# Kernel tuning notes

Hardware: AMD Instinct MI355X
Metric: run time of the kernel (lower is better)

## Reference

```python
import jax, jax.numpy as jnp
import numpy as np

NUM_NODES = 100000
NUM_RELS = 200
DIM = 128
NUM_EDGES = 600000


def setup_inputs() -> dict:
    key = jax.random.key(0)
    ks = jax.random.split(key, 12)
    xav = lambda k, shp: jax.random.uniform(k, shp, jnp.float32, -1.0, 1.0) * jnp.sqrt(6.0 / (shp[0] + shp[1]))
    return {
        'edge_index': jax.random.randint(ks[0], (2, NUM_EDGES), 0, NUM_NODES),
        'edge_type': jax.random.randint(ks[1], (NUM_EDGES,), 0, NUM_RELS),
        'edge_weight': jax.random.uniform(ks[2], (NUM_EDGES,), jnp.float32),
        'node_emb': xav(ks[3], (NUM_NODES, DIM)),
        'rel_emb': xav(ks[4], (NUM_RELS, DIM)),
        'W0': xav(ks[5], (DIM, DIM)),
        'Wself0': xav(ks[6], (DIM, DIM)),
        'Wrel0': xav(ks[7], (DIM, DIM)),
        'W1': xav(ks[8], (DIM, DIM)),
        'Wself1': xav(ks[9], (DIM, DIM)),
        'Wrel1': xav(ks[10], (DIM, DIM)),
    }


def comp_sub(x_src, r):
    return x_src - r


def compgcn_conv(x, rel, edge_index, edge_type, edge_weight, W, Wself, Wrel):
    src, dst = edge_index[0], edge_index[1]
    # edge-wise gather + composition: [E, D]
    msg = comp_sub(x[src], rel[edge_type])
    msg = msg * edge_weight[:, None]
    # scatter-add aggregation to destination nodes: [N, D]
    agg = jax.ops.segment_sum(msg, dst, num_segments=x.shape[0])
    x_out = agg @ W + x @ Wself
    rel_out = rel @ Wrel
    return x_out, rel_out


def reference(edge_index, edge_type, edge_weight, node_emb, rel_emb,
              W0, Wself0, Wrel0, W1, Wself1, Wrel1):
    # layer 0
    x, rel = compgcn_conv(node_emb, rel_emb, edge_index, edge_type, edge_weight,
                          W0, Wself0, Wrel0)
    # inter-layer nonlinearity (dropout is identity in eval mode)
    x = jax.nn.relu(x)
    rel = jax.nn.relu(rel)
    # layer 1 (last layer: no relu/dropout after)
    x, rel = compgcn_conv(x, rel, edge_index, edge_type, edge_weight,
                          W1, Wself1, Wrel1)
    return x, rel
```

## Files before the change

### kernel.cpp

```cpp
#include <hip/hip_runtime.h>

#define DD 128

typedef __attribute__((ext_vector_type(8))) short bf16x8;
typedef __attribute__((ext_vector_type(4))) float f32x4;

__device__ __forceinline__ float b2f(unsigned short u) {
    return __uint_as_float(((unsigned)u) << 16);
}
__device__ __forceinline__ unsigned short f2b(float f) {
    unsigned u = __float_as_uint(f);
    unsigned r = (u + 0x7FFFu + ((u >> 16) & 1u)) >> 16;
    return (unsigned short)r;
}


__global__ __launch_bounds__(256) void zero_kernel(int4* __restrict__ p, int n4) {
    int i = blockIdx.x * 256 + threadIdx.x;
    if (i < n4) p[i] = make_int4(0, 0, 0, 0);
}


__global__ __launch_bounds__(256) void scan1_kernel(const int* __restrict__ cnt8,
                                                    int* __restrict__ startv,
                                                    int* __restrict__ bsum, int n) {
    int i = blockIdx.x * 256 + threadIdx.x;
    int v = 0;
    if (i < n) {
#pragma unroll
        for (int p = 0; p < 8; ++p) v += cnt8[p * n + i];
    }
    int lane = threadIdx.x & 63, wid = threadIdx.x >> 6;
    int incl = v;
#pragma unroll
    for (int o = 1; o < 64; o <<= 1) {
        int t = __shfl_up(incl, o);
        if (lane >= o) incl += t;
    }
    __shared__ int wsum[4];
    __shared__ int wpre[4];
    if (lane == 63) wsum[wid] = incl;
    __syncthreads();
    if (threadIdx.x == 0) {
        int s = 0;
        for (int w2 = 0; w2 < 4; ++w2) { wpre[w2] = s; s += wsum[w2]; }
        bsum[blockIdx.x] = s;
    }
    __syncthreads();
    if (i < n) startv[i] = incl - v + wpre[wid];
}

__global__ __launch_bounds__(512) void scan2_kernel(int* bsum, int nb) {
    int i = threadIdx.x;
    int v = (i < nb) ? bsum[i] : 0;
    int lane = threadIdx.x & 63, wid = threadIdx.x >> 6;
    int incl = v;
#pragma unroll
    for (int o = 1; o < 64; o <<= 1) {
        int t = __shfl_up(incl, o);
        if (lane >= o) incl += t;
    }
    __shared__ int wsum[8];
    __shared__ int wpre[8];
    if (lane == 63) wsum[wid] = incl;
    __syncthreads();
    if (threadIdx.x == 0) {
        int s = 0;
        for (int w2 = 0; w2 < 8; ++w2) { wpre[w2] = s; s += wsum[w2]; }
    }
    __syncthreads();
    if (i < nb) bsum[i] = incl - v + wpre[wid];
}

__global__ __launch_bounds__(256) void scan3_kernel(int* startv,
                                                    const int* __restrict__ cnt8,
                                                    int* __restrict__ cursor8,
                                                    const int* __restrict__ bsum,
                                                    int n, int E) {
    int i = blockIdx.x * 256 + threadIdx.x;
    if (i < n) {
        int s = startv[i] + bsum[i >> 8];
        startv[i] = s;
        int run = s;
#pragma unroll
        for (int p = 0; p < 8; ++p) {
            cursor8[p * n + i] = run;
            run += cnt8[p * n + i];
        }
    } else if (i == n) {
        startv[n] = E;
    }
}

__global__ __launch_bounds__(256) void fill_kernel(const int* __restrict__ ei,
                                                   const int* __restrict__ ety,
                                                   const float* __restrict__ ew,
                                                   int* cursor8,
                                                   uint2* __restrict__ csre,
                                                   int E, int n) {
    int e = blockIdx.x * 256 + threadIdx.x;
    if (e >= E) return;
    int p = blockIdx.x & 7;
    int dst = ei[E + e];
    int pos = atomicAdd(&cursor8[p * n + dst], 1);
    uint2 rec;
    rec.x = ((unsigned)ei[e]) | (((unsigned)ety[e]) << 20);
    rec.y = __float_as_uint(ew[e]);
    __builtin_nontemporal_store(*(unsigned long long*)&rec,
                                (unsigned long long*)&csre[pos]);
}


__global__ __launch_bounds__(256) void prep_hist_kernel(
    const float* __restrict__ x0, unsigned short* __restrict__ xb, int bx, int n4x,
    const float* __restrict__ r0, unsigned short* __restrict__ r0b, int br, int n4r,
    const float* __restrict__ W0, const float* __restrict__ Ws0,
    const float* __restrict__ W1, const float* __restrict__ Ws1,
    const float* __restrict__ Wr0, const float* __restrict__ Wr1,
    unsigned short* __restrict__ wt0a, unsigned short* __restrict__ wt0s,
    unsigned short* __restrict__ wt1a, unsigned short* __restrict__ wt1s,
    unsigned short* __restrict__ wtr0, unsigned short* __restrict__ wtr1,
    const int* __restrict__ ei, int* __restrict__ cnt8, int E, int n) {
    int bid = blockIdx.x;
    if (bid < bx) {
        int i = bid * 256 + threadIdx.x;
        if (i < n4x) {
            float4 v = ((const float4*)x0)[i];
            ((ushort4*)xb)[i] = make_ushort4(f2b(v.x), f2b(v.y), f2b(v.z), f2b(v.w));
        }
        return;
    }
    bid -= bx;
    if (bid < br) {
        int i = bid * 256 + threadIdx.x;
        if (i < n4r) {
            float4 v = ((const float4*)r0)[i];
            ((ushort4*)r0b)[i] = make_ushort4(f2b(v.x), f2b(v.y), f2b(v.z), f2b(v.w));
        }
        return;
    }
    bid -= br;
    if (bid < 384) {
        int which = bid >> 6;
        int i = (bid & 63) * 256 + threadIdx.x;
        int cc = i >> 7, k = i & 127;
        const float* Wsel = which == 0 ? W0 : which == 1 ? Ws0 : which == 2 ? W1
                          : which == 3 ? Ws1 : which == 4 ? Wr0 : Wr1;
        unsigned short* Osel = which == 0 ? wt0a : which == 1 ? wt0s : which == 2 ? wt1a
                             : which == 3 ? wt1s : which == 4 ? wtr0 : wtr1;
        Osel[i] = f2b(Wsel[k * DD + cc]);
        return;
    }
    bid -= 384;
    int e = bid * 256 + threadIdx.x;
    if (e < E) {
        int p = bid & 7;
        atomicAdd(&cnt8[p * n + ei[E + e]], 1);
    }
}


__global__ __launch_bounds__(256) void aggregate_kernel(
    const unsigned short* __restrict__ xb, const unsigned short* __restrict__ relb,
    const int* __restrict__ startv, const uint2* __restrict__ csre,
    unsigned short* __restrict__ aggb, int n) {
    int slot = threadIdx.x >> 4;
    int c = threadIdx.x & 15;
    int n0 = blockIdx.x * 32 + slot;
    int n1 = n0 + 16;
    int i0 = 0, e0 = 0, i1 = 0, e1 = 0;
    if (n0 < n) { i0 = startv[n0]; e0 = startv[n0 + 1]; }
    if (n1 < n) { i1 = startv[n1]; e1 = startv[n1 + 1]; }
    const bf16x8* X = (const bf16x8*)xb;
    const bf16x8* Rl = (const bf16x8*)relb;
    float p0[8], q0[8], p1[8], q1[8];
#pragma unroll
    for (int j = 0; j < 8; ++j) { p0[j] = 0.f; q0[j] = 0.f; p1[j] = 0.f; q1[j] = 0.f; }
    while (i0 < e0 || i1 < e1) {
        bool v00 = i0 < e0, v01 = i0 + 1 < e0;
        bool v10 = i1 < e1, v11 = i1 + 1 < e1;
        uint2 c00 = csre[v00 ? i0 : 0];
        uint2 c01 = csre[v01 ? i0 + 1 : 0];
        uint2 c10 = csre[v10 ? i1 : 0];
        uint2 c11 = csre[v11 ? i1 + 1 : 0];
        float w00 = v00 ? __uint_as_float(c00.y) : 0.f;
        float w01 = v01 ? __uint_as_float(c01.y) : 0.f;
        float w10 = v10 ? __uint_as_float(c10.y) : 0.f;
        float w11 = v11 ? __uint_as_float(c11.y) : 0.f;
        bf16x8 x00 = X[(size_t)(c00.x & 0xFFFFFu) * 16 + c];
        bf16x8 x01 = X[(size_t)(c01.x & 0xFFFFFu) * 16 + c];
        bf16x8 x10 = X[(size_t)(c10.x & 0xFFFFFu) * 16 + c];
        bf16x8 x11 = X[(size_t)(c11.x & 0xFFFFFu) * 16 + c];
        bf16x8 r00 = Rl[(c00.x >> 20) * 16 + c];
        bf16x8 r01 = Rl[(c01.x >> 20) * 16 + c];
        bf16x8 r10 = Rl[(c10.x >> 20) * 16 + c];
        bf16x8 r11 = Rl[(c11.x >> 20) * 16 + c];
#pragma unroll
        for (int j = 0; j < 8; ++j) {
            p0[j] += (b2f((unsigned short)x00[j]) - b2f((unsigned short)r00[j])) * w00;
            q0[j] += (b2f((unsigned short)x01[j]) - b2f((unsigned short)r01[j])) * w01;
            p1[j] += (b2f((unsigned short)x10[j]) - b2f((unsigned short)r10[j])) * w10;
            q1[j] += (b2f((unsigned short)x11[j]) - b2f((unsigned short)r11[j])) * w11;
        }
        i0 = min(i0 + 2, e0);
        i1 = min(i1 + 2, e1);
    }
    if (n0 < n) {
        bf16x8 ov;
#pragma unroll
        for (int j = 0; j < 8; ++j) ov[j] = (short)f2b(p0[j] + q0[j]);
        ((bf16x8*)aggb)[(size_t)n0 * 16 + c] = ov;
    }
    if (n1 < n) {
        bf16x8 ov;
#pragma unroll
        for (int j = 0; j < 8; ++j) ov[j] = (short)f2b(p1[j] + q1[j]);
        ((bf16x8*)aggb)[(size_t)n1 * 16 + c] = ov;
    }
}


__global__ __launch_bounds__(512, 4) void mfma_dual_gemm_kernel(
    const unsigned short* __restrict__ A, const unsigned short* __restrict__ X,
    const unsigned short* __restrict__ WtA, const unsigned short* __restrict__ WtX,
    float* __restrict__ outf, unsigned short* __restrict__ outb,
    int nrows, int relu,
    const unsigned short* __restrict__ relsrc, const unsigned short* __restrict__ WtR,
    float* __restrict__ reloutf, unsigned short* __restrict__ reloutb,
    int R, int gbl) {
    __shared__ unsigned short sW[2][DD * DD];
    bool isrel = (int)blockIdx.x >= gbl;
    const unsigned short* srcA = isrel ? WtR : WtA;
    for (int i = threadIdx.x; i < 2048; i += 512) {
        int row = i >> 4, slot = i & 15;
        int so = (slot ^ (row & 15)) * 8;
        *(float4*)&sW[0][row * DD + so] = ((const float4*)srcA)[i];
        *(float4*)&sW[1][row * DD + so] = ((const float4*)WtX)[i];
    }
    __syncthreads();
    int w = threadIdx.x >> 6, l = threadIdx.x & 63;
    int lr = l & 15, lk = l >> 4;

    f32x4 acc[8];
#pragma unroll
    for (int ct = 0; ct < 8; ++ct) acc[ct] = (f32x4){0.f, 0.f, 0.f, 0.f};

    if (!isrel) {
        int row = blockIdx.x * 128 + w * 16 + lr;
        bool v = row < nrows;
#pragma unroll
        for (int kb = 0; kb < 4; ++kb) {
            int koff = kb * 32 + lk * 8;
            bf16x8 a = {}, x = {};
            if (v) {
                a = *(const bf16x8*)(A + (size_t)row * DD + koff);
                x = *(const bf16x8*)(X + (size_t)row * DD + koff);
            }
#pragma unroll
            for (int ct = 0; ct < 8; ++ct) {
                int wrow = ct * 16 + lr;
                int slot = kb * 4 + lk;
                int so = (slot ^ (wrow & 15)) * 8;
                bf16x8 bw = *(const bf16x8*)&sW[0][wrow * DD + so];
                bf16x8 bs = *(const bf16x8*)&sW[1][wrow * DD + so];
                acc[ct] = __builtin_amdgcn_mfma_f32_16x16x32_bf16(bw, a, acc[ct], 0, 0, 0);
                acc[ct] = __builtin_amdgcn_mfma_f32_16x16x32_bf16(bs, x, acc[ct], 0, 0, 0);
            }
        }
        if (v) {
#pragma unroll
            for (int ct = 0; ct < 8; ++ct) {
                f32x4 vv = acc[ct];
                if (relu) {
                    vv[0] = fmaxf(vv[0], 0.f); vv[1] = fmaxf(vv[1], 0.f);
                    vv[2] = fmaxf(vv[2], 0.f); vv[3] = fmaxf(vv[3], 0.f);
                }
                int cb = ct * 16 + lk * 4;
                if (outf) *(f32x4*)(outf + (size_t)row * DD + cb) = vv;
                if (outb) {
                    *(ushort4*)(outb + (size_t)row * DD + cb) =
                        make_ushort4(f2b(vv[0]), f2b(vv[1]), f2b(vv[2]), f2b(vv[3]));
                }
            }
        }
    } else {
        int row = ((int)blockIdx.x - gbl) * 128 + w * 16 + lr;
        bool v = row < R;
#pragma unroll
        for (int kb = 0; kb < 4; ++kb) {
            int koff = kb * 32 + lk * 8;
            bf16x8 a = {};
            if (v) a = *(const bf16x8*)(relsrc + (size_t)row * DD + koff);
#pragma unroll
            for (int ct = 0; ct < 8; ++ct) {
                int wrow = ct * 16 + lr;
                int slot = kb * 4 + lk;
                int so = (slot ^ (wrow & 15)) * 8;
                bf16x8 bw = *(const bf16x8*)&sW[0][wrow * DD + so];
                acc[ct] = __builtin_amdgcn_mfma_f32_16x16x32_bf16(bw, a, acc[ct], 0, 0, 0);
            }
        }
        if (v) {
#pragma unroll
            for (int ct = 0; ct < 8; ++ct) {
                f32x4 vv = acc[ct];
                if (relu) {
                    vv[0] = fmaxf(vv[0], 0.f); vv[1] = fmaxf(vv[1], 0.f);
                    vv[2] = fmaxf(vv[2], 0.f); vv[3] = fmaxf(vv[3], 0.f);
                }
                int cb = ct * 16 + lk * 4;
                if (reloutf) *(f32x4*)(reloutf + (size_t)row * DD + cb) = vv;
                if (reloutb) {
                    *(ushort4*)(reloutb + (size_t)row * DD + cb) =
                        make_ushort4(f2b(vv[0]), f2b(vv[1]), f2b(vv[2]), f2b(vv[3]));
                }
            }
        }
    }
}


extern "C" void kernel_launch(void* const* d_in, const int* in_sizes, int n_in,
                              void* d_out, int out_size, void* d_ws, size_t ws_size,
                              hipStream_t stream) {
    const int*   ei  = (const int*)d_in[0];
    const int*   ety = (const int*)d_in[1];
    const float* ew  = (const float*)d_in[2];
    const float* x0  = (const float*)d_in[3];
    const float* r0  = (const float*)d_in[4];
    const float* W0  = (const float*)d_in[5];
    const float* Ws0 = (const float*)d_in[6];
    const float* Wr0 = (const float*)d_in[7];
    const float* W1  = (const float*)d_in[8];
    const float* Ws1 = (const float*)d_in[9];
    const float* Wr1 = (const float*)d_in[10];

    const int E = in_sizes[1];
    const int N = in_sizes[3] / DD;
    const int R = in_sizes[4] / DD;

    float* out_x = (float*)d_out;
    float* out_r = out_x + (size_t)N * DD;

    char* w = (char*)d_ws;
    size_t off = 0;
    auto alloc = [&](size_t bytes) {
        void* p = w + off;
        off += (bytes + 255) & ~(size_t)255;
        return p;
    };
    unsigned short* aggb  = (unsigned short*)alloc((size_t)N * DD * 2);
    unsigned short* xb    = (unsigned short*)alloc((size_t)N * DD * 2);
    unsigned short* r0b   = (unsigned short*)alloc((size_t)R * DD * 2);
    unsigned short* rel1b = (unsigned short*)alloc((size_t)R * DD * 2);
    unsigned short* wt0a  = (unsigned short*)alloc((size_t)DD * DD * 2);
    unsigned short* wt0s  = (unsigned short*)alloc((size_t)DD * DD * 2);
    unsigned short* wt1a  = (unsigned short*)alloc((size_t)DD * DD * 2);
    unsigned short* wt1s  = (unsigned short*)alloc((size_t)DD * DD * 2);
    unsigned short* wtr0  = (unsigned short*)alloc((size_t)DD * DD * 2);
    unsigned short* wtr1  = (unsigned short*)alloc((size_t)DD * DD * 2);
    int*   startv = (int*)alloc((size_t)(N + 1) * 4);
    int*   bsum   = (int*)alloc(512 * 4);
    uint2* csre   = (uint2*)alloc((size_t)E * 8);
    (void)ws_size; (void)n_in; (void)out_size;

    int* cnt8    = (int*)aggb;
    int* cursor8 = cnt8 + (size_t)8 * N;

    int ebl = (E + 255) / 256;
    int nb  = (N + 255) / 256;
    int n4x = N * 32, n4r = R * 32;
    int bx = (n4x + 255) / 256, br = (n4r + 255) / 256;

    zero_kernel<<<(2 * N + 255) / 256, 256, 0, stream>>>((int4*)cnt8, 2 * N);

    prep_hist_kernel<<<bx + br + 384 + ebl, 256, 0, stream>>>(
        x0, xb, bx, n4x, r0, r0b, br, n4r,
        W0, Ws0, W1, Ws1, Wr0, Wr1,
        wt0a, wt0s, wt1a, wt1s, wtr0, wtr1, ei, cnt8, E, N);
    scan1_kernel<<<nb, 256, 0, stream>>>(cnt8, startv, bsum, N);
    scan2_kernel<<<1, 512, 0, stream>>>(bsum, nb);
    scan3_kernel<<<(N + 1 + 255) / 256, 256, 0, stream>>>(startv, cnt8, cursor8,
                                                          bsum, N, E);
    fill_kernel<<<ebl, 256, 0, stream>>>(ei, ety, ew, cursor8, csre, E, N);

    int abl = (N + 31) / 32;
    int gbl = (N + 127) / 128;
    int rblk = (R + 127) / 128;

    aggregate_kernel<<<abl, 256, 0, stream>>>(xb, r0b, startv, csre, aggb, N);
    mfma_dual_gemm_kernel<<<gbl + rblk, 512, 0, stream>>>(
        aggb, xb, wt0a, wt0s, nullptr, xb, N, 1,
        r0b, wtr0, nullptr, rel1b, R, gbl);

    aggregate_kernel<<<abl, 256, 0, stream>>>(xb, rel1b, startv, csre, aggb, N);
    mfma_dual_gemm_kernel<<<gbl + rblk, 512, 0, stream>>>(
        aggb, xb, wt1a, wt1s, out_x, nullptr, N, 0,
        rel1b, wtr1, out_r, nullptr, R, gbl);
}
```

Before: 208.8 us.

## Bucket CSR edges partition-major, then compact into node-contiguous order

Edge records are now placed partition-major: a scan over all 8×N partition counts gives each (partition, node) its own contiguous range. A new compact kernel then gathers these ranges into one node-contiguous CSR array, which the aggregation kernels read. The aim is to make the fill kernel's scattered writes more local and to cut conflicts between partitions. The cost is an extra pass and an extra E×8-byte buffer. The histogram blocks are moved to the front of the prep kernel, and the fill store is no longer nontemporal.

```diff
diff --git a/kernel.cpp b/kernel.cpp
--- a/kernel.cpp
+++ b/kernel.cpp
@@ -1,6 +1,7 @@
 #include <hip/hip_runtime.h>
 
 #define DD 128
+#define NP 8
 
 typedef __attribute__((ext_vector_type(8))) short bf16x8;
 typedef __attribute__((ext_vector_type(4))) float f32x4;
@@ -21,16 +22,80 @@
 }
 
 
-__global__ __launch_bounds__(256) void scan1_kernel(const int* __restrict__ cnt8,
-                                                    int* __restrict__ startv,
-                                                    int* __restrict__ bsum, int n) {
-    int i = blockIdx.x * 256 + threadIdx.x;
-    int v = 0;
-    if (i < n) {
-#pragma unroll
-        for (int p = 0; p < 8; ++p) v += cnt8[p * n + i];
-    }
-    int lane = threadIdx.x & 63, wid = threadIdx.x >> 6;
+__global__ __launch_bounds__(256) void prep_hist_kernel(
+    const int* __restrict__ ei, int* __restrict__ cnt8, int E, int ebl, int n,
+    const float* __restrict__ x0, unsigned short* __restrict__ xb, int bx, int n4x,
+    const float* __restrict__ r0, unsigned short* __restrict__ r0b, int br, int n4r,
+    const float* __restrict__ W0, const float* __restrict__ Ws0,
+    const float* __restrict__ W1, const float* __restrict__ Ws1,
+    const float* __restrict__ Wr0, const float* __restrict__ Wr1,
+    unsigned short* __restrict__ wt0a, unsigned short* __restrict__ wt0s,
+    unsigned short* __restrict__ wt1a, unsigned short* __restrict__ wt1s,
+    unsigned short* __restrict__ wtr0, unsigned short* __restrict__ wtr1) {
+    int bid = blockIdx.x;
+    if (bid < ebl) {
+        int e = bid * 256 + threadIdx.x;
+        if (e < E) {
+            int p = bid & (NP - 1);
+            atomicAdd(&cnt8[p * n + ei[E + e]], 1);
+        }
+        return;
+    }
+    bid -= ebl;
+    if (bid < bx) {
+        int i = bid * 256 + threadIdx.x;
+        if (i < n4x) {
+            float4 v = ((const float4*)x0)[i];
+            ((ushort4*)xb)[i] = make_ushort4(f2b(v.x), f2b(v.y), f2b(v.z), f2b(v.w));
+        }
+        return;
+    }
+    bid -= bx;
+    if (bid < br) {
+        int i = bid * 256 + threadIdx.x;
+        if (i < n4r) {
+            float4 v = ((const float4*)r0)[i];
+            ((ushort4*)r0b)[i] = make_ushort4(f2b(v.x), f2b(v.y), f2b(v.z), f2b(v.w));
+        }
+        return;
+    }
+    bid -= br;
+    int which = bid >> 6;
+    int i = (bid & 63) * 256 + threadIdx.x;
+    int cc = i >> 7, k = i & 127;
+    const float* Wsel = which == 0 ? W0 : which == 1 ? Ws0 : which == 2 ? W1
+                      : which == 3 ? Ws1 : which == 4 ? Wr0 : Wr1;
+    unsigned short* Osel = which == 0 ? wt0a : which == 1 ? wt0s : which == 2 ? wt1a
+                         : which == 3 ? wt1s : which == 4 ? wtr0 : wtr1;
+    Osel[i] = f2b(Wsel[k * DD + cc]);
+}
+
+
+__global__ __launch_bounds__(256) void scan1_kernel(
+    const int* __restrict__ cnt8, int* __restrict__ start8, int* __restrict__ bsum8,
+    int n8, int nb8, int* __restrict__ startv, int* __restrict__ bsumb, int n) {
+    int bid = blockIdx.x;
+    int tid = threadIdx.x;
+    int idx, v;
+    int* outp;
+    int* bsump;
+    if (bid < nb8) {
+        idx = bid * 256 + tid;
+        v = (idx < n8) ? cnt8[idx] : 0;
+        outp = start8;
+        bsump = bsum8 + bid;
+    } else {
+        int b2 = bid - nb8;
+        idx = b2 * 256 + tid;
+        v = 0;
+        if (idx < n) {
+#pragma unroll
+            for (int p = 0; p < NP; ++p) v += cnt8[p * n + idx];
+        }
+        outp = startv;
+        bsump = bsumb + b2;
+    }
+    int lane = tid & 63, wid = tid >> 6;
     int incl = v;
 #pragma unroll
     for (int o = 1; o < 64; o <<= 1) {
@@ -41,55 +106,68 @@
     __shared__ int wpre[4];
     if (lane == 63) wsum[wid] = incl;
     __syncthreads();
-    if (threadIdx.x == 0) {
+    if (tid == 0) {
         int s = 0;
         for (int w2 = 0; w2 < 4; ++w2) { wpre[w2] = s; s += wsum[w2]; }
-        bsum[blockIdx.x] = s;
+        *bsump = s;
     }
     __syncthreads();
-    if (i < n) startv[i] = incl - v + wpre[wid];
-}
-
-__global__ __launch_bounds__(512) void scan2_kernel(int* bsum, int nb) {
-    int i = threadIdx.x;
-    int v = (i < nb) ? bsum[i] : 0;
-    int lane = threadIdx.x & 63, wid = threadIdx.x >> 6;
-    int incl = v;
-#pragma unroll
-    for (int o = 1; o < 64; o <<= 1) {
-        int t = __shfl_up(incl, o);
-        if (lane >= o) incl += t;
-    }
+    bool valid = (bid < nb8) ? (idx < n8) : (idx < n);
+    if (valid) outp[idx] = incl - v + wpre[wid];
+}
+
+__global__ __launch_bounds__(512) void scan2_kernel(int* bsum8, int nb8,
+                                                    int* bsumb, int nb) {
+    int tid = threadIdx.x, lane = tid & 63, wid = tid >> 6;
     __shared__ int wsum[8];
     __shared__ int wpre[8];
-    if (lane == 63) wsum[wid] = incl;
+    __shared__ int carry, tot;
+    int* arr = (blockIdx.x == 0) ? bsum8 : bsumb;
+    int cnt = (blockIdx.x == 0) ? nb8 : nb;
+    if (tid == 0) carry = 0;
     __syncthreads();
-    if (threadIdx.x == 0) {
-        int s = 0;
-        for (int w2 = 0; w2 < 8; ++w2) { wpre[w2] = s; s += wsum[w2]; }
-    }
-    __syncthreads();
-    if (i < nb) bsum[i] = incl - v + wpre[wid];
-}
-
-__global__ __launch_bounds__(256) void scan3_kernel(int* startv,
-                                                    const int* __restrict__ cnt8,
-                                                    int* __restrict__ cursor8,
-                                                    const int* __restrict__ bsum,
-                                                    int n, int E) {
-    int i = blockIdx.x * 256 + threadIdx.x;
-    if (i < n) {
-        int s = startv[i] + bsum[i >> 8];
-        startv[i] = s;
-        int run = s;
-#pragma unroll
-        for (int p = 0; p < 8; ++p) {
-            cursor8[p * n + i] = run;
-            run += cnt8[p * n + i];
-        }
-    } else if (i == n) {
-        startv[n] = E;
-    }
+    for (int base = 0; base < cnt; base += 512) {
+        int i = base + tid;
+        int v = (i < cnt) ? arr[i] : 0;
+        int incl = v;
+#pragma unroll
+        for (int o = 1; o < 64; o <<= 1) {
+            int t = __shfl_up(incl, o);
+            if (lane >= o) incl += t;
+        }
+        if (lane == 63) wsum[wid] = incl;
+        __syncthreads();
+        if (tid == 0) {
+            int s = 0;
+            for (int w2 = 0; w2 < 8; ++w2) { wpre[w2] = s; s += wsum[w2]; }
+            tot = s;
+        }
+        __syncthreads();
+        if (i < cnt) arr[i] = incl - v + wpre[wid] + carry;
+        __syncthreads();
+        if (tid == 0) carry += tot;
+        __syncthreads();
+    }
+}
+
+__global__ __launch_bounds__(256) void scan3_kernel(
+    int* __restrict__ start8, int* __restrict__ cursor8,
+    const int* __restrict__ bsum8, int n8, int nb8,
+    int* __restrict__ startv, const int* __restrict__ bsumb, int n, int E) {
+    int bid = blockIdx.x;
+    if (bid < nb8) {
+        int i = bid * 256 + threadIdx.x;
+        if (i < n8) {
+            int s = start8[i] + bsum8[bid];
+            start8[i] = s;
+            cursor8[i] = s;
+        }
+        return;
+    }
+    int b2 = bid - nb8;
+    int i = b2 * 256 + threadIdx.x;
+    if (i < n) startv[i] += bsumb[b2];
+    else if (i == n) startv[n] = E;
 }
 
 __global__ __launch_bounds__(256) void fill_kernel(const int* __restrict__ ei,
@@ -100,62 +178,27 @@
                                                    int E, int n) {
     int e = blockIdx.x * 256 + threadIdx.x;
     if (e >= E) return;
-    int p = blockIdx.x & 7;
+    int p = blockIdx.x & (NP - 1);
     int dst = ei[E + e];
     int pos = atomicAdd(&cursor8[p * n + dst], 1);
     uint2 rec;
     rec.x = ((unsigned)ei[e]) | (((unsigned)ety[e]) << 20);
     rec.y = __float_as_uint(ew[e]);
-    __builtin_nontemporal_store(*(unsigned long long*)&rec,
-                                (unsigned long long*)&csre[pos]);
-}
-
-
-__global__ __launch_bounds__(256) void prep_hist_kernel(
-    const float* __restrict__ x0, unsigned short* __restrict__ xb, int bx, int n4x,
-    const float* __restrict__ r0, unsigned short* __restrict__ r0b, int br, int n4r,
-    const float* __restrict__ W0, const float* __restrict__ Ws0,
-    const float* __restrict__ W1, const float* __restrict__ Ws1,
-    const float* __restrict__ Wr0, const float* __restrict__ Wr1,
-    unsigned short* __restrict__ wt0a, unsigned short* __restrict__ wt0s,
-    unsigned short* __restrict__ wt1a, unsigned short* __restrict__ wt1s,
-    unsigned short* __restrict__ wtr0, unsigned short* __restrict__ wtr1,
-    const int* __restrict__ ei, int* __restrict__ cnt8, int E, int n) {
-    int bid = blockIdx.x;
-    if (bid < bx) {
-        int i = bid * 256 + threadIdx.x;
-        if (i < n4x) {
-            float4 v = ((const float4*)x0)[i];
-            ((ushort4*)xb)[i] = make_ushort4(f2b(v.x), f2b(v.y), f2b(v.z), f2b(v.w));
-        }
-        return;
-    }
-    bid -= bx;
-    if (bid < br) {
-        int i = bid * 256 + threadIdx.x;
-        if (i < n4r) {
-            float4 v = ((const float4*)r0)[i];
-            ((ushort4*)r0b)[i] = make_ushort4(f2b(v.x), f2b(v.y), f2b(v.z), f2b(v.w));
-        }
-        return;
-    }
-    bid -= br;
-    if (bid < 384) {
-        int which = bid >> 6;
-        int i = (bid & 63) * 256 + threadIdx.x;
-        int cc = i >> 7, k = i & 127;
-        const float* Wsel = which == 0 ? W0 : which == 1 ? Ws0 : which == 2 ? W1
-                          : which == 3 ? Ws1 : which == 4 ? Wr0 : Wr1;
-        unsigned short* Osel = which == 0 ? wt0a : which == 1 ? wt0s : which == 2 ? wt1a
-                             : which == 3 ? wt1s : which == 4 ? wtr0 : wtr1;
-        Osel[i] = f2b(Wsel[k * DD + cc]);
-        return;
-    }
-    bid -= 384;
-    int e = bid * 256 + threadIdx.x;
-    if (e < E) {
-        int p = bid & 7;
-        atomicAdd(&cnt8[p * n + ei[E + e]], 1);
+    csre[pos] = rec;
+}
+
+__global__ __launch_bounds__(256) void compact_kernel(
+    const uint2* __restrict__ csre, const int* __restrict__ start8,
+    const int* __restrict__ cursor8, const int* __restrict__ startv,
+    uint2* __restrict__ csre2, int n) {
+    int i = blockIdx.x * 256 + threadIdx.x;
+    if (i >= n) return;
+    int base = startv[i];
+#pragma unroll
+    for (int p = 0; p < NP; ++p) {
+        int s = start8[p * n + i];
+        int e = cursor8[p * n + i];
+        for (int k = s; k < e; ++k) csre2[base++] = csre[k];
     }
 }
 
@@ -360,40 +403,48 @@
     unsigned short* wtr0  = (unsigned short*)alloc((size_t)DD * DD * 2);
     unsigned short* wtr1  = (unsigned short*)alloc((size_t)DD * DD * 2);
     int*   startv = (int*)alloc((size_t)(N + 1) * 4);
-    int*   bsum   = (int*)alloc(512 * 4);
+    int*   bsum8  = (int*)alloc(3328 * 4);
+    int*   bsumb  = (int*)alloc(512 * 4);
     uint2* csre   = (uint2*)alloc((size_t)E * 8);
+    uint2* csre2  = (uint2*)alloc((size_t)E * 8);
     (void)ws_size; (void)n_in; (void)out_size;
 
     int* cnt8    = (int*)aggb;
-    int* cursor8 = cnt8 + (size_t)8 * N;
+    int* start8  = cnt8 + (size_t)NP * N;
+    int* cursor8 = start8 + (size_t)NP * N;
 
     int ebl = (E + 255) / 256;
+    int n8  = NP * N;
+    int nb8 = (n8 + 255) / 256;
     int nb  = (N + 255) / 256;
+    int nbp1 = (N + 1 + 255) / 256;
     int n4x = N * 32, n4r = R * 32;
     int bx = (n4x + 255) / 256, br = (n4r + 255) / 256;
 
-    zero_kernel<<<(2 * N + 255) / 256, 256, 0, stream>>>((int4*)cnt8, 2 * N);
-
-    prep_hist_kernel<<<bx + br + 384 + ebl, 256, 0, stream>>>(
+    zero_kernel<<<(n8 / 4 + 255) / 256, 256, 0, stream>>>((int4*)cnt8, n8 / 4);
+    prep_hist_kernel<<<ebl + bx + br + 384, 256, 0, stream>>>(
+        ei, cnt8, E, ebl, N,
         x0, xb, bx, n4x, r0, r0b, br, n4r,
         W0, Ws0, W1, Ws1, Wr0, Wr1,
-        wt0a, wt0s, wt1a, wt1s, wtr0, wtr1, ei, cnt8, E, N);
-    scan1_kernel<<<nb, 256, 0, stream>>>(cnt8, startv, bsum, N);
-    scan2_kernel<<<1, 512, 0, stream>>>(bsum, nb);
-    scan3_kernel<<<(N + 1 + 255) / 256, 256, 0, stream>>>(startv, cnt8, cursor8,
-                                                          bsum, N, E);
+        wt0a, wt0s, wt1a, wt1s, wtr0, wtr1);
+    scan1_kernel<<<nb8 + nb, 256, 0, stream>>>(cnt8, start8, bsum8, n8, nb8,
+                                               startv, bsumb, N);
+    scan2_kernel<<<2, 512, 0, stream>>>(bsum8, nb8, bsumb, nb);
+    scan3_kernel<<<nb8 + nbp1, 256, 0, stream>>>(start8, cursor8, bsum8, n8, nb8,
+                                                 startv, bsumb, N, E);
     fill_kernel<<<ebl, 256, 0, stream>>>(ei, ety, ew, cursor8, csre, E, N);
+    compact_kernel<<<nb, 256, 0, stream>>>(csre, start8, cursor8, startv, csre2, N);
 
     int abl = (N + 31) / 32;
     int gbl = (N + 127) / 128;
     int rblk = (R + 127) / 128;
 
-    aggregate_kernel<<<abl, 256, 0, stream>>>(xb, r0b, startv, csre, aggb, N);
+    aggregate_kernel<<<abl, 256, 0, stream>>>(xb, r0b, startv, csre2, aggb, N);
     mfma_dual_gemm_kernel<<<gbl + rblk, 512, 0, stream>>>(
         aggb, xb, wt0a, wt0s, nullptr, xb, N, 1,
         r0b, wtr0, nullptr, rel1b, R, gbl);
 
-    aggregate_kernel<<<abl, 256, 0, stream>>>(xb, rel1b, startv, csre, aggb, N);
+    aggregate_kernel<<<abl, 256, 0, stream>>>(xb, rel1b, startv, csre2, aggb, N);
     mfma_dual_gemm_kernel<<<gbl + rblk, 512, 0, stream>>>(
         aggb, xb, wt1a, wt1s, out_x, nullptr, N, 0,
         rel1b, wtr1, out_r, nullptr, R, gbl);
```

New measurement: 213.6 us. 2.3% more time.
